# Optimization experiments

Hardware: AMD Instinct MI355X
Metric: run time of the kernel (lower is better)

## Reference

```python
import jax, jax.numpy as jnp
import numpy as np

B, NQ, NK, D, DV = 8, 2048, 2048, 64, 64
MASK_VAL = -1e9  # any value < -1.0 triggers substitution in the original t.where


def setup_inputs() -> dict:
    key = jax.random.key(0)
    kq, kk, kv = jax.random.split(key, 3)
    queries = jax.random.normal(kq, (B, NQ, D), dtype=jnp.float32)
    keys = jax.random.normal(kk, (B, NK, D), dtype=jnp.float32)
    values = jax.random.normal(kv, (B, NK, DV), dtype=jnp.float32)
    # causal-style substitution mask: 0.0 where attended, -1e9 where masked
    causal = jnp.tril(jnp.ones((NQ, NK), dtype=jnp.float32))
    mask2d = jnp.where(causal > 0, 0.0, MASK_VAL)
    attention_mask = jnp.broadcast_to(mask2d, (B, NQ, NK))
    return {"queries": queries, "keys": keys, "values": values,
            "attention_mask": attention_mask}


def reference(queries, keys, values, attention_mask):
    # logits = Q K^T / sqrt(d_k)
    d_k = keys.shape[-1]
    scale = jnp.asarray(1.0 / np.sqrt(d_k), dtype=queries.dtype)
    logits = jnp.einsum('bqd,bkd->bqk', queries, keys) * scale
    # substitution masking: replace logits by the mask VALUE where mask < -1.0
    masked = jnp.where(attention_mask < -1.0, attention_mask, logits)
    attn = jax.nn.softmax(masked, axis=-1)
    # post-hoc NaN zeroing (rows fully masked with -inf would be NaN)
    attn = jnp.where(jnp.isnan(attn), jnp.asarray(0.0, attn.dtype), attn)
    return jnp.einsum('bqk,bkv->bqv', attn, values)
```

## Files before the change

### kernel.cpp

```cpp
#include <hip/hip_runtime.h>

#define NB    8
#define NQL   2048
#define NKL   2048
#define DD    64
#define DVV   64
#define QT    128
#define NQT   16
#define CHK   256
#define MAXCH 8
#define KSTEP 64

typedef __attribute__((ext_vector_type(8))) short bf16x8;
typedef __attribute__((ext_vector_type(4))) short bf16x4;
typedef __attribute__((ext_vector_type(2))) short bf16x2;
typedef __attribute__((ext_vector_type(4))) float f32x4;

#define L2E 1.44269504088896340736f

__device__ __forceinline__ unsigned short f2bf(float x) {
    union { float f; unsigned u; } v; v.f = x;
    unsigned r = v.u + 0x7FFFu + ((v.u >> 16) & 1u);
    return (unsigned short)(r >> 16);
}

__device__ __forceinline__ int kswz(int row, int col) {
    return row * 64 + (col ^ ((row & 7) << 3));
}
__device__ __forceinline__ int vswz(int dv, int col) {
    return dv * 64 + (col ^ ((((dv & 7) ^ ((dv >> 3) & 7))) << 3));
}

__global__ __launch_bounds__(512, 4)
void attn_part(const float* __restrict__ Qg, const float* __restrict__ Kg,
               const float* __restrict__ Vg, float* __restrict__ Og,
               float* __restrict__ Mp, float* __restrict__ Lp,
               float* __restrict__ Op)
{
    const int bid = blockIdx.x;
    const int kc  = bid & 7;
    const int qt  = (bid >> 3) & 15;
    const int b   = bid >> 7;
    const int nkeys = QT * (qt + 1);
    const int KC0   = kc * CHK;
    if (KC0 >= nkeys) return;
    const int nsteps = (min(nkeys - KC0, CHK)) >> 6;
    const int nch    = (qt + 2) >> 1;
    const int tile   = b * NQT + qt;

    const int tid  = threadIdx.x;
    const int wv   = tid >> 6;
    const int lane = tid & 63;
    const int c    = lane & 15;
    const int h    = lane >> 4;
    const int Q0   = qt * QT;
    const int R0l  = 16 * wv;

    const float* Qb = Qg + (size_t)b * NQL * DD;
    const float* Kb = Kg + (size_t)b * NKL * DD;
    const float* Vb = Vg + (size_t)b * NKL * DVV;

    __shared__ __align__(16) char smem[36864];
    short (*Kl)[4096] = (short (*)[4096])smem;
    short (*Vl)[4096] = (short (*)[4096])(smem + 16384);
    float (*Ot)[68]   = (float (*)[68])smem;
    float* Mr   = (float*)(smem + 34816);
    float* Lr   = Mr + 128;
    float* invb = Lr + 128;

    const int skr = tid >> 3;
    const int sdc = (tid & 7) * 8;
    const int vkr = (tid >> 4) << 1;
    const int vdc = (tid & 15) * 4;
    f32x4 kr[2], vr[2];

    bf16x8 qf[2];
#pragma unroll
    for (int dh = 0; dh < 2; ++dh) {
        const float* src = Qb + (size_t)(Q0 + R0l + c) * DD + dh * 32 + h * 8;
        f32x4 x0 = *(const f32x4*)(src);
        f32x4 x1 = *(const f32x4*)(src + 4);
        bf16x8 t;
#pragma unroll
        for (int j = 0; j < 4; ++j) {
            t[j]     = (short)f2bf(x0[j] * 0.125f);
            t[4 + j] = (short)f2bf(x1[j] * 0.125f);
        }
        qf[dh] = t;
    }

    {
        const float* kb0 = Kb + (size_t)(KC0 + skr) * DD + sdc;
        kr[0] = *(const f32x4*)(kb0); kr[1] = *(const f32x4*)(kb0 + 4);
        const float* vb0 = Vb + (size_t)(KC0 + vkr) * DVV + vdc;
        vr[0] = *(const f32x4*)(vb0); vr[1] = *(const f32x4*)(vb0 + DVV);
        short* Kd = Kl[0]; short* Vd = Vl[0];
#pragma unroll
        for (int i = 0; i < 2; ++i) {
            bf16x4 t;
#pragma unroll
            for (int j = 0; j < 4; ++j) t[j] = (short)f2bf(kr[i][j]);
            *(bf16x4*)(Kd + kswz(skr, sdc + 4 * i)) = t;
        }
#pragma unroll
        for (int j = 0; j < 4; ++j) {
            bf16x2 t;
            t[0] = (short)f2bf(vr[0][j]);
            t[1] = (short)f2bf(vr[1][j]);
            *(bf16x2*)(Vd + vswz(vdc + j, vkr)) = t;
        }
    }
    __syncthreads();

    float m = -INFINITY, l = 0.0f;
    f32x4 acc[4];
    {
        f32x4 z = {0.f, 0.f, 0.f, 0.f};
#pragma unroll
        for (int s4 = 0; s4 < 4; ++s4) acc[s4] = z;
    }

    for (int s = 0; s < nsteps; ++s) {
        const int pb = s & 1;

        if (s + 1 < nsteps) {
            const float* kb0 = Kb + (size_t)(KC0 + (s + 1) * KSTEP + skr) * DD + sdc;
            kr[0] = *(const f32x4*)(kb0); kr[1] = *(const f32x4*)(kb0 + 4);
            const float* vb0 = Vb + (size_t)(KC0 + (s + 1) * KSTEP + vkr) * DVV + vdc;
            vr[0] = *(const f32x4*)(vb0); vr[1] = *(const f32x4*)(vb0 + DVV);
        }

        const int kg0 = KC0 + s * KSTEP;
        if (kg0 <= Q0 + R0l + 15) {
            const short* Kd = Kl[pb];
            const short* Vd = Vl[pb];

            f32x4 st[4];
            {
                f32x4 z = {0.f, 0.f, 0.f, 0.f};
#pragma unroll
                for (int t = 0; t < 4; ++t) st[t] = z;
            }
#pragma unroll
            for (int t = 0; t < 4; ++t)
#pragma unroll
                for (int dh = 0; dh < 2; ++dh) {
                    bf16x8 kf = *(const bf16x8*)(Kd + kswz(16 * t + c, dh * 32 + h * 8));
                    st[t] = __builtin_amdgcn_mfma_f32_16x16x32_bf16(kf, qf[dh], st[t], 0, 0, 0);
                }

            if (kg0 + KSTEP - 1 > Q0 + R0l) {
                const int qg = Q0 + R0l + c;
#pragma unroll
                for (int t = 0; t < 4; ++t)
#pragma unroll
                    for (int r = 0; r < 4; ++r) {
                        int key = kg0 + 16 * t + 4 * h + r;
                        if (key > qg) st[t][r] = -1e9f;
                    }
            }

            float vmax = st[0][0];
#pragma unroll
            for (int t = 0; t < 4; ++t)
#pragma unroll
                for (int r = 0; r < 4; ++r) vmax = fmaxf(vmax, st[t][r]);
            vmax = fmaxf(vmax, __shfl_xor(vmax, 16));
            vmax = fmaxf(vmax, __shfl_xor(vmax, 32));

            if (!__all(vmax - m <= 8.0f)) {
                float mn    = fmaxf(m, vmax);
                float alpha = exp2f((m - mn) * L2E);
                l *= alpha;
#pragma unroll
                for (int s4 = 0; s4 < 4; ++s4)
#pragma unroll
                    for (int r = 0; r < 4; ++r) acc[s4][r] *= alpha;
                m = mn;
            }

            float p[4][4];
            float ps = 0.f;
#pragma unroll
            for (int t = 0; t < 4; ++t)
#pragma unroll
                for (int r = 0; r < 4; ++r) {
                    p[t][r] = exp2f((st[t][r] - m) * L2E);
                    ps += p[t][r];
                }
            ps += __shfl_xor(ps, 16);
            ps += __shfl_xor(ps, 32);
            l += ps;

            bf16x8 pf[2];
#pragma unroll
            for (int u = 0; u < 2; ++u) {
                bf16x8 t;
#pragma unroll
                for (int j = 0; j < 8; ++j) t[j] = (short)f2bf(p[2 * u + (j >> 2)][j & 3]);
                pf[u] = t;
            }
#pragma unroll
            for (int s4 = 0; s4 < 4; ++s4)
#pragma unroll
                for (int u = 0; u < 2; ++u) {
                    bf16x4 lo = *(const bf16x4*)(Vd + vswz(c + 16 * s4, 32 * u + 4 * h));
                    bf16x4 hi = *(const bf16x4*)(Vd + vswz(c + 16 * s4, 32 * u + 16 + 4 * h));
                    bf16x8 vf = {lo[0], lo[1], lo[2], lo[3], hi[0], hi[1], hi[2], hi[3]};
                    acc[s4] = __builtin_amdgcn_mfma_f32_16x16x32_bf16(vf, pf[u], acc[s4], 0, 0, 0);
                }
        }

        if (s + 1 < nsteps) {
            short* Kd = Kl[(s + 1) & 1];
            short* Vd = Vl[(s + 1) & 1];
#pragma unroll
            for (int i = 0; i < 2; ++i) {
                bf16x4 t;
#pragma unroll
                for (int j = 0; j < 4; ++j) t[j] = (short)f2bf(kr[i][j]);
                *(bf16x4*)(Kd + kswz(skr, sdc + 4 * i)) = t;
            }
#pragma unroll
            for (int j = 0; j < 4; ++j) {
                bf16x2 t;
                t[0] = (short)f2bf(vr[0][j]);
                t[1] = (short)f2bf(vr[1][j]);
                *(bf16x2*)(Vd + vswz(vdc + j, vkr)) = t;
            }
        }
        __syncthreads();
    }

#pragma unroll
    for (int s4 = 0; s4 < 4; ++s4)
        *(f32x4*)&Ot[R0l + c][16 * s4 + 4 * h] = acc[s4];
    if (h == 0) { Mr[R0l + c] = m; Lr[R0l + c] = l; }
    __syncthreads();

    float* Ogb = Og + ((size_t)b * NQL + Q0) * DVV;

    if (nch == 1) {
        if (tid < 128) invb[tid] = 1.0f / Lr[tid];
        __syncthreads();
#pragma unroll
        for (int j = 0; j < 16; ++j) {
            int f = j * 512 + tid;
            Ogb[f] = Ot[f >> 6][f & 63] * invb[f >> 6];
        }
        return;
    }

    float* Opg = Op + ((size_t)tile * MAXCH + kc) * (QT * DVV);
#pragma unroll
    for (int j = 0; j < 16; ++j) {
        int f = j * 512 + tid;
        Opg[f] = Ot[f >> 6][f & 63];
    }
    if (tid < 128) {
        Mp[((size_t)tile * MAXCH + kc) * QT + tid] = Mr[tid];
        Lp[((size_t)tile * MAXCH + kc) * QT + tid] = Lr[tid];
    }
}

__global__ __launch_bounds__(256)
void attn_comb(const float* __restrict__ Op, const float* __restrict__ Mp,
               const float* __restrict__ Lp, float* __restrict__ Og)
{
    const int seg  = blockIdx.x & 3;
    const int tile = blockIdx.x >> 2;
    const int qt   = tile & 15;
    const int b    = tile >> 4;
    const int nch  = (qt + 2) >> 1;
    if (nch == 1) return;

    const int tid = threadIdx.x;
    const int r0  = seg * 32;

    __shared__ float scb[MAXCH][32];

    if (tid < 32) {
        const int row = r0 + tid;
        float M = -INFINITY;
        for (int ch = 0; ch < nch; ++ch)
            M = fmaxf(M, Mp[((size_t)tile * MAXCH + ch) * QT + row]);
        float den = 0.f;
        for (int ch = 0; ch < nch; ++ch) {
            float e = exp2f((Mp[((size_t)tile * MAXCH + ch) * QT + row] - M) * L2E);
            den += e * Lp[((size_t)tile * MAXCH + ch) * QT + row];
            scb[ch][tid] = e;
        }
        float iv = 1.0f / den;
        for (int ch = 0; ch < nch; ++ch) scb[ch][tid] *= iv;
    }
    __syncthreads();

    const float* Opt = Op + (size_t)tile * MAXCH * (QT * DVV) + r0 * DVV;
    float* dst = Og + ((size_t)b * NQL + qt * QT + r0) * DVV;
#pragma unroll
    for (int j = 0; j < 8; ++j) {
        int f = j * 256 + tid;
        int row = f >> 6;
        float val = 0.f;
        for (int ch = 0; ch < nch; ++ch)
            val += scb[ch][row] * Opt[(size_t)ch * (QT * DVV) + f];
        dst[f] = val;
    }
}

__global__ __launch_bounds__(256, 4)
void attn_fwd_fb(const float* __restrict__ Qg, const float* __restrict__ Kg,
                 const float* __restrict__ Vg, float* __restrict__ Og)
{
    const int tid  = threadIdx.x;
    const int wv   = tid >> 6;
    const int lane = tid & 63;
    const int c    = lane & 15;
    const int h    = lane >> 4;
    const int bid = blockIdx.x;
    const int b   = bid & 7;
    const int qt  = bid >> 3;
    const int q0  = qt << 4;
    const float* Qb = Qg + (size_t)b * NQL * DD;
    const float* Kb = Kg + (size_t)b * NKL * DD;
    const float* Vb = Vg + (size_t)b * NKL * DVV;
    bf16x8 qf[2];
#pragma unroll
    for (int dh = 0; dh < 2; ++dh) {
        const float* src = Qb + (size_t)(q0 + c) * DD + dh * 32 + h * 8;
        f32x4 x0 = *(const f32x4*)(src);
        f32x4 x1 = *(const f32x4*)(src + 4);
        bf16x8 t;
#pragma unroll
        for (int j = 0; j < 4; ++j) {
            t[j]     = (short)f2bf(x0[j] * 0.125f);
            t[4 + j] = (short)f2bf(x1[j] * 0.125f);
        }
        qf[dh] = t;
    }
    float m = -INFINITY, l = 0.0f;
    f32x4 acc[4];
    {
        f32x4 z = {0.f, 0.f, 0.f, 0.f};
#pragma unroll
        for (int s = 0; s < 4; ++s) acc[s] = z;
    }
    const int nkt = (q0 + 47) >> 5;
    for (int kt = wv; kt < nkt; kt += 4) {
        const int kb = kt << 5;
        f32x4 st[2];
        {
            f32x4 z = {0.f, 0.f, 0.f, 0.f};
            st[0] = z; st[1] = z;
        }
#pragma unroll
        for (int t = 0; t < 2; ++t)
#pragma unroll
            for (int dh = 0; dh < 2; ++dh) {
                const float* src = Kb + (size_t)(kb + t * 16 + c) * DD + dh * 32 + h * 8;
                f32x4 x0 = *(const f32x4*)(src);
                f32x4 x1 = *(const f32x4*)(src + 4);
                bf16x8 kf;
#pragma unroll
                for (int j = 0; j < 4; ++j) {
                    kf[j]     = (short)f2bf(x0[j]);
                    kf[4 + j] = (short)f2bf(x1[j]);
                }
                st[t] = __builtin_amdgcn_mfma_f32_16x16x32_bf16(kf, qf[dh], st[t], 0, 0, 0);
            }
        if (kb + 31 > q0) {
#pragma unroll
            for (int t = 0; t < 2; ++t)
#pragma unroll
                for (int r = 0; r < 4; ++r) {
                    int key = kb + t * 16 + h * 4 + r;
                    if (key > q0 + c) st[t][r] = -1e9f;
                }
        }
        float vmax = st[0][0];
#pragma unroll
        for (int t = 0; t < 2; ++t)
#pragma unroll
            for (int r = 0; r < 4; ++r) vmax = fmaxf(vmax, st[t][r]);
        vmax = fmaxf(vmax, __shfl_xor(vmax, 16));
        vmax = fmaxf(vmax, __shfl_xor(vmax, 32));
        float mn    = fmaxf(m, vmax);
        float alpha = exp2f((m - mn) * L2E);
        float p[2][4];
        float ps = 0.f;
#pragma unroll
        for (int t = 0; t < 2; ++t)
#pragma unroll
            for (int r = 0; r < 4; ++r) {
                p[t][r] = exp2f((st[t][r] - mn) * L2E);
                ps += p[t][r];
            }
        ps += __shfl_xor(ps, 16);
        ps += __shfl_xor(ps, 32);
        l = l * alpha + ps;
        m = mn;
#pragma unroll
        for (int s = 0; s < 4; ++s)
#pragma unroll
            for (int r = 0; r < 4; ++r) acc[s][r] *= alpha;
        bf16x8 pf;
#pragma unroll
        for (int j = 0; j < 8; ++j) pf[j] = (short)f2bf(p[j >> 2][j & 3]);
        size_t vrow[8];
#pragma unroll
        for (int j = 0; j < 8; ++j)
            vrow[j] = (size_t)(kb + h * 4 + (j & 3) + ((j >> 2) << 4)) * DVV + c;
#pragma unroll
        for (int s = 0; s < 4; ++s) {
            bf16x8 vf;
#pragma unroll
            for (int j = 0; j < 8; ++j) vf[j] = (short)f2bf(Vb[vrow[j] + s * 16]);
            acc[s] = __builtin_amdgcn_mfma_f32_16x16x32_bf16(vf, pf, acc[s], 0, 0, 0);
        }
    }
    __shared__ float Osc[4][64][17];
    __shared__ float Msc[4][16];
    __shared__ float Lsc[4][16];
#pragma unroll
    for (int s = 0; s < 4; ++s)
#pragma unroll
        for (int r = 0; r < 4; ++r)
            Osc[wv][s * 16 + h * 4 + r][c] = acc[s][r];
    if (lane < 16) { Msc[wv][c] = m; Lsc[wv][c] = l; }
    __syncthreads();
#pragma unroll
    for (int ri = 0; ri < 4; ++ri) {
        const int q = wv * 4 + ri;
        float M = fmaxf(fmaxf(Msc[0][q], Msc[1][q]), fmaxf(Msc[2][q], Msc[3][q]));
        float val = 0.f, den = 0.f;
#pragma unroll
        for (int w2 = 0; w2 < 4; ++w2) {
            float sc = exp2f((Msc[w2][q] - M) * L2E);
            den += Lsc[w2][q] * sc;
            val += Osc[w2][lane][q] * sc;
        }
        Og[((size_t)b * NQL + q0 + q) * DVV + lane] = val / den;
    }
}

extern "C" void kernel_launch(void* const* d_in, const int* in_sizes, int n_in,
                              void* d_out, int out_size, void* d_ws, size_t ws_size,
                              hipStream_t stream)
{
    (void)in_sizes; (void)n_in; (void)out_size;
    const float* Q = (const float*)d_in[0];
    const float* K = (const float*)d_in[1];
    const float* V = (const float*)d_in[2];
    float* O = (float*)d_out;

    const size_t ml_elems = (size_t)(NB * NQT) * MAXCH * QT;
    const size_t op_elems = (size_t)(NB * NQT) * MAXCH * QT * DVV;
    const size_t need = (2 * ml_elems + op_elems) * sizeof(float);

    if (ws_size >= need) {
        float* Mp = (float*)d_ws;
        float* Lp = Mp + ml_elems;
        float* Op = Lp + ml_elems;
        attn_part<<<dim3(NB * NQT * MAXCH), dim3(512), 0, stream>>>(
            Q, K, V, O, Mp, Lp, Op);
        attn_comb<<<dim3(NB * NQT * 4), dim3(256), 0, stream>>>(Op, Mp, Lp, O);
    } else {
        attn_fwd_fb<<<dim3(NB * (NQL / 16)), dim3(256), 0, stream>>>(Q, K, V, O);
    }
}
```

Before: 56.39 us.

## Halve query tile, compact causal grid with paired chunk scheduling, write partials directly

Shrinks the query tile from 128 to 64 rows with 256-thread blocks. The grid becomes a compact 1152-block launch that pairs light and heavy key-chunk workloads, so no block exits early on the causal mask. Partial outputs and the single-chunk normalized output are now written straight from registers instead of staging through shared memory. The combine kernel is remapped to the new tile count. This aims to cut wasted blocks and even out load, at the cost of more partial tiles to combine and more per-thread load registers.

```diff
diff --git a/kernel.cpp b/kernel.cpp
--- a/kernel.cpp
+++ b/kernel.cpp
@@ -5,8 +5,8 @@
 #define NKL   2048
 #define DD    64
 #define DVV   64
-#define QT    128
-#define NQT   16
+#define QT    64
+#define NQT   32
 #define CHK   256
 #define MAXCH 8
 #define KSTEP 64
@@ -31,21 +31,28 @@
     return dv * 64 + (col ^ ((((dv & 7) ^ ((dv >> 3) & 7))) << 3));
 }
 
-__global__ __launch_bounds__(512, 4)
+__global__ __launch_bounds__(256, 4)
 void attn_part(const float* __restrict__ Qg, const float* __restrict__ Kg,
                const float* __restrict__ Vg, float* __restrict__ Og,
                float* __restrict__ Mp, float* __restrict__ Lp,
                float* __restrict__ Op)
 {
-    const int bid = blockIdx.x;
-    const int kc  = bid & 7;
-    const int qt  = (bid >> 3) & 15;
-    const int b   = bid >> 7;
-    const int nkeys = QT * (qt + 1);
-    const int KC0   = kc * CHK;
-    if (KC0 >= nkeys) return;
-    const int nsteps = (min(nkeys - KC0, CHK)) >> 6;
-    const int nch    = (qt + 2) >> 1;
+    const int x    = blockIdx.x & 7;
+    const int slot = blockIdx.x >> 3;
+    const int a_cnt = 128 - 16 * x;
+    int kc, b, qt;
+    if (slot < a_cnt) {
+        const int w = 32 - 4 * x;
+        kc = x;      b = slot / w;           qt = 4 * x + slot % w;
+    } else {
+        const int s2 = slot - a_cnt;
+        const int w = 4 + 4 * x;
+        kc = 7 - x;  b = 4 + s2 / w;         qt = 4 * (7 - x) + s2 % w;
+    }
+    const int nkeys  = QT * (qt + 1);
+    const int KC0    = kc * CHK;
+    const int nsteps = min(4, (nkeys - KC0) >> 6);
+    const int nch    = (qt + 4) >> 2;
     const int tile   = b * NQT + qt;
 
     const int tid  = threadIdx.x;
@@ -60,19 +67,14 @@
     const float* Kb = Kg + (size_t)b * NKL * DD;
     const float* Vb = Vg + (size_t)b * NKL * DVV;
 
-    __shared__ __align__(16) char smem[36864];
-    short (*Kl)[4096] = (short (*)[4096])smem;
-    short (*Vl)[4096] = (short (*)[4096])(smem + 16384);
-    float (*Ot)[68]   = (float (*)[68])smem;
-    float* Mr   = (float*)(smem + 34816);
-    float* Lr   = Mr + 128;
-    float* invb = Lr + 128;
-
-    const int skr = tid >> 3;
-    const int sdc = (tid & 7) * 8;
-    const int vkr = (tid >> 4) << 1;
-    const int vdc = (tid & 15) * 4;
-    f32x4 kr[2], vr[2];
+    __shared__ short Kl[2][64 * 64];
+    __shared__ short Vl[2][64 * 64];
+
+    const int skr = tid >> 2;
+    const int sdc = (tid & 3) * 16;
+    const int vkr = (tid >> 3) << 1;
+    const int vdc = (tid & 7) * 8;
+    f32x4 kr[4], vr[4];
 
     bf16x8 qf[2];
 #pragma unroll
@@ -91,22 +93,24 @@
 
     {
         const float* kb0 = Kb + (size_t)(KC0 + skr) * DD + sdc;
-        kr[0] = *(const f32x4*)(kb0); kr[1] = *(const f32x4*)(kb0 + 4);
+        kr[0] = *(const f32x4*)(kb0);     kr[1] = *(const f32x4*)(kb0 + 4);
+        kr[2] = *(const f32x4*)(kb0 + 8); kr[3] = *(const f32x4*)(kb0 + 12);
         const float* vb0 = Vb + (size_t)(KC0 + vkr) * DVV + vdc;
-        vr[0] = *(const f32x4*)(vb0); vr[1] = *(const f32x4*)(vb0 + DVV);
+        vr[0] = *(const f32x4*)(vb0);       vr[1] = *(const f32x4*)(vb0 + 4);
+        vr[2] = *(const f32x4*)(vb0 + DVV); vr[3] = *(const f32x4*)(vb0 + DVV + 4);
         short* Kd = Kl[0]; short* Vd = Vl[0];
 #pragma unroll
-        for (int i = 0; i < 2; ++i) {
+        for (int i = 0; i < 4; ++i) {
             bf16x4 t;
 #pragma unroll
             for (int j = 0; j < 4; ++j) t[j] = (short)f2bf(kr[i][j]);
             *(bf16x4*)(Kd + kswz(skr, sdc + 4 * i)) = t;
         }
 #pragma unroll
-        for (int j = 0; j < 4; ++j) {
+        for (int j = 0; j < 8; ++j) {
             bf16x2 t;
-            t[0] = (short)f2bf(vr[0][j]);
-            t[1] = (short)f2bf(vr[1][j]);
+            t[0] = (short)f2bf(vr[j >> 2][j & 3]);
+            t[1] = (short)f2bf(vr[2 + (j >> 2)][j & 3]);
             *(bf16x2*)(Vd + vswz(vdc + j, vkr)) = t;
         }
     }
@@ -125,9 +129,11 @@
 
         if (s + 1 < nsteps) {
             const float* kb0 = Kb + (size_t)(KC0 + (s + 1) * KSTEP + skr) * DD + sdc;
-            kr[0] = *(const f32x4*)(kb0); kr[1] = *(const f32x4*)(kb0 + 4);
+            kr[0] = *(const f32x4*)(kb0);     kr[1] = *(const f32x4*)(kb0 + 4);
+            kr[2] = *(const f32x4*)(kb0 + 8); kr[3] = *(const f32x4*)(kb0 + 12);
             const float* vb0 = Vb + (size_t)(KC0 + (s + 1) * KSTEP + vkr) * DVV + vdc;
-            vr[0] = *(const f32x4*)(vb0); vr[1] = *(const f32x4*)(vb0 + DVV);
+            vr[0] = *(const f32x4*)(vb0);       vr[1] = *(const f32x4*)(vb0 + 4);
+            vr[2] = *(const f32x4*)(vb0 + DVV); vr[3] = *(const f32x4*)(vb0 + DVV + 4);
         }
 
         const int kg0 = KC0 + s * KSTEP;
@@ -215,51 +221,44 @@
             short* Kd = Kl[(s + 1) & 1];
             short* Vd = Vl[(s + 1) & 1];
 #pragma unroll
-            for (int i = 0; i < 2; ++i) {
+            for (int i = 0; i < 4; ++i) {
                 bf16x4 t;
 #pragma unroll
                 for (int j = 0; j < 4; ++j) t[j] = (short)f2bf(kr[i][j]);
                 *(bf16x4*)(Kd + kswz(skr, sdc + 4 * i)) = t;
             }
 #pragma unroll
-            for (int j = 0; j < 4; ++j) {
+            for (int j = 0; j < 8; ++j) {
                 bf16x2 t;
-                t[0] = (short)f2bf(vr[0][j]);
-                t[1] = (short)f2bf(vr[1][j]);
+                t[0] = (short)f2bf(vr[j >> 2][j & 3]);
+                t[1] = (short)f2bf(vr[2 + (j >> 2)][j & 3]);
                 *(bf16x2*)(Vd + vswz(vdc + j, vkr)) = t;
             }
         }
         __syncthreads();
     }
 
+    const int q = R0l + c;
+    if (nch == 1) {
+        const float iv = 1.0f / l;
+        float* dst = Og + ((size_t)b * NQL + Q0 + q) * DVV;
+#pragma unroll
+        for (int s4 = 0; s4 < 4; ++s4) {
+            f32x4 t = acc[s4];
+#pragma unroll
+            for (int r = 0; r < 4; ++r) t[r] *= iv;
+            *(f32x4*)(dst + 16 * s4 + 4 * h) = t;
+        }
+        return;
+    }
+
+    float* Opg = Op + ((size_t)tile * MAXCH + kc) * (QT * DVV);
 #pragma unroll
     for (int s4 = 0; s4 < 4; ++s4)
-        *(f32x4*)&Ot[R0l + c][16 * s4 + 4 * h] = acc[s4];
-    if (h == 0) { Mr[R0l + c] = m; Lr[R0l + c] = l; }
-    __syncthreads();
-
-    float* Ogb = Og + ((size_t)b * NQL + Q0) * DVV;
-
-    if (nch == 1) {
-        if (tid < 128) invb[tid] = 1.0f / Lr[tid];
-        __syncthreads();
-#pragma unroll
-        for (int j = 0; j < 16; ++j) {
-            int f = j * 512 + tid;
-            Ogb[f] = Ot[f >> 6][f & 63] * invb[f >> 6];
-        }
-        return;
-    }
-
-    float* Opg = Op + ((size_t)tile * MAXCH + kc) * (QT * DVV);
-#pragma unroll
-    for (int j = 0; j < 16; ++j) {
-        int f = j * 512 + tid;
-        Opg[f] = Ot[f >> 6][f & 63];
-    }
-    if (tid < 128) {
-        Mp[((size_t)tile * MAXCH + kc) * QT + tid] = Mr[tid];
-        Lp[((size_t)tile * MAXCH + kc) * QT + tid] = Lr[tid];
+        *(f32x4*)(Opg + (size_t)q * DVV + 16 * s4 + 4 * h) = acc[s4];
+    if (h == 0) {
+        Mp[((size_t)tile * MAXCH + kc) * QT + q] = m;
+        Lp[((size_t)tile * MAXCH + kc) * QT + q] = l;
     }
 }
 
@@ -267,11 +266,11 @@
 void attn_comb(const float* __restrict__ Op, const float* __restrict__ Mp,
                const float* __restrict__ Lp, float* __restrict__ Og)
 {
-    const int seg  = blockIdx.x & 3;
-    const int tile = blockIdx.x >> 2;
-    const int qt   = tile & 15;
-    const int b    = tile >> 4;
-    const int nch  = (qt + 2) >> 1;
+    const int seg  = blockIdx.x & 1;
+    const int tile = blockIdx.x >> 1;
+    const int qt   = tile & (NQT - 1);
+    const int b    = tile >> 5;
+    const int nch  = (qt + 4) >> 2;
     if (nch == 1) return;
 
     const int tid = threadIdx.x;
@@ -295,7 +294,7 @@
     }
     __syncthreads();
 
-    const float* Opt = Op + (size_t)tile * MAXCH * (QT * DVV) + r0 * DVV;
+    const float* Opt = Op + (size_t)tile * MAXCH * (QT * DVV) + (size_t)r0 * DVV;
     float* dst = Og + ((size_t)b * NQL + qt * QT + r0) * DVV;
 #pragma unroll
     for (int j = 0; j < 8; ++j) {
@@ -461,9 +460,8 @@
         float* Mp = (float*)d_ws;
         float* Lp = Mp + ml_elems;
         float* Op = Lp + ml_elems;
-        attn_part<<<dim3(NB * NQT * MAXCH), dim3(512), 0, stream>>>(
-            Q, K, V, O, Mp, Lp, Op);
-        attn_comb<<<dim3(NB * NQT * 4), dim3(256), 0, stream>>>(Op, Mp, Lp, O);
+        attn_part<<<dim3(1152), dim3(256), 0, stream>>>(Q, K, V, O, Mp, Lp, Op);
+        attn_comb<<<dim3(NB * NQT * 2), dim3(256), 0, stream>>>(Op, Mp, Lp, O);
     } else {
         attn_fwd_fb<<<dim3(NB * (NQL / 16)), dim3(256), 0, stream>>>(Q, K, V, O);
     }
```

New measurement: 50.22 us. -10.9%, faster.
